# Optimization experiments

Hardware: AMD Instinct MI355X
Metric: run time of the kernel (lower is better)

The kernel has to match this reference:

```python
import jax, jax.numpy as jnp
import numpy as np

T, B, A, N = 64, 32, 8, 16
E, H = 64, 4
LSTM_I, LSTM_H = 128, 128
D_SELF = 16 + 9 * (32 - 2) + 4  # 290


def setup_inputs() -> dict:
    key = jax.random.key(0)
    ks = jax.random.split(key, 24)
    f32 = jnp.float32
    d = {}
    d["x_agent"] = jax.random.normal(ks[0], (T, B, A, 16), f32)
    d["x_lidar"] = jax.random.normal(ks[1], (T, B, A, 32), f32)
    d["x_safe_zone"] = jax.random.normal(ks[2], (T, B, A, 4), f32)
    d["x_ent0"] = jax.random.normal(ks[3], (T, B, A, N, 12), f32)
    d["x_ent1"] = jax.random.normal(ks[4], (T, B, A, N, 8), f32)
    d["mask0"] = jax.random.randint(ks[5], (T, B, A, N), 0, 2).astype(jnp.int32)
    d["mask1"] = jax.random.randint(ks[6], (T, B, A, N), 0, 2).astype(jnp.int32)
    d["done"] = jax.random.randint(ks[7], (T, B), 0, 2).astype(jnp.int32)
    d["actions"] = jax.random.randint(ks[8], (T, B, A, 2), 0, 5).astype(jnp.int32)
    w = lambda k, s: jax.random.normal(k, s, f32) * 0.05
    z = lambda s: jnp.zeros(s, f32)
    d["conv_w"] = w(ks[9], (9, 1, 3)); d["conv_b"] = z((9,))
    d["self_w"] = w(ks[10], (E, 2 * D_SELF)); d["self_b"] = z((E,))
    d["ent0_w"] = w(ks[11], (E, 12 + D_SELF)); d["ent0_b"] = z((E,))
    d["ent1_w"] = w(ks[12], (E, 8 + D_SELF)); d["ent1_b"] = z((E,))
    d["in_proj_w"] = w(ks[13], (3 * E, E)); d["in_proj_b"] = z((3 * E,))
    d["out_proj_w"] = w(ks[14], (E, E)); d["out_proj_b"] = z((E,))
    d["sa_w"] = w(ks[15], (E, E)); d["sa_b"] = z((E,))
    d["pool_w"] = w(ks[16], (LSTM_I, D_SELF + E)); d["pool_b"] = z((LSTM_I,))
    d["w_ih"] = w(ks[17], (4 * LSTM_H, LSTM_I)); d["w_hh"] = w(ks[18], (4 * LSTM_H, LSTM_H))
    d["b_ih"] = z((4 * LSTM_H,)); d["b_hh"] = z((4 * LSTM_H,))
    d["head0_w"] = w(ks[19], (5, LSTM_H)); d["head0_b"] = z((5,))
    d["head1_w"] = w(ks[20], (5, LSTM_H)); d["head1_b"] = z((5,))
    return d


def _forward(x_agent, x_lidar, x_safe_zone, x_ent0, x_ent1,
             conv_w, conv_b, self_w, self_b, ent0_w, ent0_b, ent1_w, ent1_b,
             in_proj_w, in_proj_b, out_proj_w, out_proj_b, sa_w, sa_b,
             pool_w, pool_b, w_ih, w_hh, b_ih, b_hh,
             head0_w, head0_b, head1_w, head1_b,
             mask0, mask1, done, actions):
    f32 = jnp.float32
    lin = lambda x, w, b: x @ w.T + b
    # lidar conv: Conv1d(1,9,k=3), padding=0 (padding_mode='circular' is inert with padding=0)
    xl = x_lidar.reshape(T * B * A, 1, 32)
    zl = jax.lax.conv_general_dilated(xl, conv_w, (1,), 'VALID',
                                      dimension_numbers=('NCH', 'OIH', 'NCH'))
    zl = jax.nn.relu(zl + conv_b[None, :, None]).reshape(T, B, A, -1)  # (T,B,A,270)
    x_self = jnp.concatenate([x_agent, zl, x_safe_zone], axis=-1)  # (T,B,A,290)
    z_self = jax.nn.relu(lin(jnp.concatenate([x_self, x_self], -1), self_w, self_b))[..., None, :]
    xs = jnp.broadcast_to(x_self[..., None, :], (T, B, A, N, D_SELF))
    z0 = jax.nn.relu(lin(jnp.concatenate([x_ent0, xs], -1), ent0_w, ent0_b))
    z1 = jax.nn.relu(lin(jnp.concatenate([x_ent1, xs], -1), ent1_w, ent1_b))
    z_ent = jnp.concatenate([z_self, z0, z1], axis=-2)  # (T,B,A,M,E), M = 1+2N = 33
    M = z_ent.shape[-2]
    mask = jnp.concatenate([jnp.ones((T, B, A, 1), f32),
                            mask0.astype(f32), mask1.astype(f32)], axis=-1)  # (T,B,A,M)
    # self-attention over entities, flattened over (T,B,A)
    S = T * B * A
    zf = z_ent.reshape(S, M, E)
    q, k, v = jnp.split(zf @ in_proj_w.T + in_proj_b, 3, axis=-1)
    Dh = E // H
    q = q.reshape(S, M, H, Dh); k = k.reshape(S, M, H, Dh); v = v.reshape(S, M, H, Dh)
    sc = jnp.einsum('sqhd,skhd->shqk', q, k) / np.float32(np.sqrt(Dh))
    valid = mask.reshape(S, M) > 0
    sc = jnp.where(valid[:, None, None, :], sc, jnp.float32(-1e9))
    attn = jax.nn.softmax(sc, axis=-1)
    o = jnp.einsum('shqk,skhd->sqhd', attn, v).reshape(S, M, E)
    o = (o @ out_proj_w.T + out_proj_b).reshape(T, B, A, M, E)
    res = z_ent + jax.nn.relu(lin(o, sa_w, sa_b))
    z_pool = jnp.mean(res * mask[..., None], axis=-2)  # torch.mean over entity dim (divide by M)
    zin = jax.nn.relu(lin(jnp.concatenate([x_self, z_pool], -1), pool_w, pool_b))  # (T,B,A,128)
    # LSTM scan with done-based state resets (PyTorch gate order i,f,g,o)
    zin_f = zin.reshape(T, B * A, LSTM_I)
    done_f = jnp.repeat(done.astype(f32), A, axis=-1)  # (T, B*A)
    def step(carry, inp):
        h, c = carry
        x_t, d_t = inp
        keep = (1.0 - d_t)[:, None]
        h = h * keep
        c = c * keep
        g = x_t @ w_ih.T + b_ih + h @ w_hh.T + b_hh
        i, f, gg, og = jnp.split(g, 4, axis=-1)
        c = jax.nn.sigmoid(f) * c + jax.nn.sigmoid(i) * jnp.tanh(gg)
        h = jax.nn.sigmoid(og) * jnp.tanh(c)
        return (h, c), h
    h0 = jnp.zeros((B * A, LSTM_H), f32)
    c0 = jnp.zeros((B * A, LSTM_H), f32)
    _, hs = jax.lax.scan(step, (h0, c0), (zin_f, done_f))
    z_lstm = hs.reshape(T, B, A, LSTM_H)
    # categorical heads: per-head logprob of given action and entropy
    lps, ents = [], []
    for i, (hw, hb) in enumerate(((head0_w, head0_b), (head1_w, head1_b))):
        logp = jax.nn.log_softmax(lin(z_lstm, hw, hb), axis=-1)
        p = jnp.exp(logp)
        ents.append(-(p * logp).sum(-1))
        lps.append(jnp.take_along_axis(logp, actions[..., i:i + 1], axis=-1)[..., 0])
    logprobs = lps[0] * lps[1]  # .prod(dim=-1) over heads as in source
    entropies = jnp.stack(ents, axis=-1)
    return logprobs, entropies


def reference(x_agent, x_lidar, x_safe_zone, x_ent0, x_ent1, mask0, mask1, done, actions,
              conv_w, conv_b, self_w, self_b, ent0_w, ent0_b, ent1_w, ent1_b,
              in_proj_w, in_proj_b, out_proj_w, out_proj_b, sa_w, sa_b,
              pool_w, pool_b, w_ih, w_hh, b_ih, b_hh,
              head0_w, head0_b, head1_w, head1_b):
    logprobs, entropies = _forward(x_agent, x_lidar, x_safe_zone, x_ent0, x_ent1,
                                   conv_w, conv_b, self_w, self_b, ent0_w, ent0_b,
                                   ent1_w, ent1_b, in_proj_w, in_proj_b, out_proj_w,
                                   out_proj_b, sa_w, sa_b, pool_w, pool_b,
                                   w_ih, w_hh, b_ih, b_hh,
                                   head0_w, head0_b, head1_w, head1_b,
                                   mask0, mask1, done, actions)
    return (actions, logprobs, entropies)
```

## Files before the change

### kernel.cpp

```cpp
#include <hip/hip_runtime.h>
#include <hip/hip_bf16.h>
#include <math.h>

#define T_DIM 64
#define B_DIM 32
#define S_TOT 16384
#define BA 256
#define FN_SB 16

#define ACT_OFF 0
#define LP_OFF 32768
#define ENT_OFF 49152

typedef __attribute__((ext_vector_type(8))) short short8;
typedef __attribute__((ext_vector_type(4))) float f32x4;
typedef unsigned int uint32;

__device__ __forceinline__ float sigf(float x) { return 1.0f / (1.0f + expf(-x)); }
__device__ __forceinline__ float bf2f(unsigned short u) {
    union { unsigned int i; float f; } a; a.i = ((unsigned int)u) << 16; return a.f;
}
__device__ __forceinline__ uint32 pkbf(float a, float b) {
    __hip_bfloat16 ha = __float2bfloat16(a), hb = __float2bfloat16(b);
    return (uint32)(*(unsigned short*)&ha) | ((uint32)(*(unsigned short*)&hb) << 16);
}
__device__ __forceinline__ short f2bs(float v) {
    __hip_bfloat16 h = __float2bfloat16(v); return *(short*)&h;
}
__device__ __forceinline__ int pswz(int row) { return (((row & 3) ^ ((row >> 2) & 3)) << 4); }

__global__ __launch_bounds__(256) void k_cvt2(
    const float* __restrict__ inp_w, const float* __restrict__ outp_w,
    const float* __restrict__ outp_b, const float* __restrict__ sa_w,
    const float* __restrict__ sa_b, const float* __restrict__ self_w,
    const float* __restrict__ pool_w, const float* __restrict__ ent0_w,
    const float* __restrict__ ent1_w, const float* __restrict__ w_ih,
    const float* __restrict__ w_hh,
    short* __restrict__ wq, short* __restrict__ Wf,
    short* __restrict__ We0, short* __restrict__ We1,
    short* __restrict__ wos, float* __restrict__ bos,
    short* __restrict__ wihb, short* __restrict__ whhb)
{
    int i = blockIdx.x * 256 + threadIdx.x;
    if (i < 12288) wq[i] = f2bs(inp_w[i]);
    if (i < 65536) { wihb[i] = f2bs(w_ih[i]); whhb[i] = f2bs(w_hh[i]); }
    if (i < 4096) {
        int c = i >> 6, k = i & 63;
        float s = 0.f;
        for (int j = 0; j < 64; ++j) s = fmaf(sa_w[c * 64 + j], outp_w[j * 64 + k], s);
        wos[i] = f2bs(s);
    }
    if (i < 64) {
        float s = sa_b[i];
        for (int j = 0; j < 64; ++j) s = fmaf(sa_w[i * 64 + j], outp_b[j], s);
        bos[i] = s;
    }
    if (i < 1024) {
        int e = i >> 4, k = i & 15;
        We0[i] = f2bs(k < 12 ? ent0_w[e * 302 + k] : 0.f);
        We1[i] = f2bs(k < 8 ? ent1_w[e * 298 + k] : 0.f);
    }
    if (i < 102400) {
        int c = i / 320, k = i - c * 320;
        float v = 0.f;
        if (k < 290) {
            if (c < 64) v = self_w[c * 580 + k] + self_w[c * 580 + 290 + k];
            else if (c < 192) v = pool_w[(size_t)(c - 64) * 354 + k];
            else if (c < 256) v = ent0_w[(c - 192) * 302 + 12 + k];
            else v = ent1_w[(c - 256) * 298 + 8 + k];
        }
        Wf[i] = f2bs(v);
    }
}

#define FN_XSB 0
#define FN_XP0 16384
#define FN_XP1 20736
#define FN_TOTAL 25088

__global__ __launch_bounds__(256, 4) void k_frontN(
    const float* __restrict__ xag, const float* __restrict__ xlid,
    const float* __restrict__ xsz, const float* __restrict__ xe0,
    const float* __restrict__ xe1,
    const float* __restrict__ conv_w, const float* __restrict__ conv_b,
    const float* __restrict__ self_b, const float* __restrict__ ent0_b,
    const float* __restrict__ ent1_b,
    const short* __restrict__ Wf, const short* __restrict__ We0,
    const short* __restrict__ We1,
    __hip_bfloat16* __restrict__ z_ent, float* __restrict__ zin_x)
{
    extern __shared__ char smem[];
    char* xsb = smem + FN_XSB;
    float* xp0f = (float*)(smem + FN_XP0);
    float* xp1f = (float*)(smem + FN_XP1);
    char* ae = smem + FN_XSB;
    float* lidf = (float*)(smem + FN_XP0);

    const int tid = threadIdx.x;
    const int s0 = blockIdx.x * FN_SB;
    const int wv = __builtin_amdgcn_readfirstlane(tid >> 6);
    const int l = tid & 63;
    const int lr = l & 15;
    const int lg = l >> 4;

    for (int i = tid; i < FN_SB * 32; i += 256) {
        int d = i & 31, sl = i >> 5;
        lidf[d * 18 + sl] = xlid[(size_t)s0 * 32 + i];
    }
    for (int i = tid; i < FN_SB * 16; i += 256) {
        int sl = i >> 4, d = i & 15;
        *(short*)(xsb + ((sl * 640 + d * 2) ^ ((sl & 7) << 4))) = f2bs(xag[(size_t)s0 * 16 + i]);
    }
    for (int i = tid; i < FN_SB * 4; i += 256) {
        int sl = i >> 2, d = i & 3;
        *(short*)(xsb + ((sl * 640 + (286 + d) * 2) ^ ((sl & 7) << 4))) = f2bs(xsz[(size_t)s0 * 4 + i]);
    }
    for (int i = tid; i < FN_SB * 30; i += 256) {
        int sl = i / 30, d = 290 + (i - (i / 30) * 30);
        *(short*)(xsb + ((sl * 640 + d * 2) ^ ((sl & 7) << 4))) = 0;
    }
    __syncthreads();
    for (int i = tid; i < 270 * FN_SB; i += 256) {
        int cp = i >> 4, sl = i & 15;
        int c = cp / 30, p = cp - c * 30;
        float v = conv_b[c] + conv_w[c * 3] * lidf[p * 18 + sl]
                + conv_w[c * 3 + 1] * lidf[(p + 1) * 18 + sl]
                + conv_w[c * 3 + 2] * lidf[(p + 2) * 18 + sl];
        *(short*)(xsb + ((sl * 640 + (16 + cp) * 2) ^ ((sl & 7) << 4))) = f2bs(fmaxf(v, 0.f));
    }
    __syncthreads();

    f32x4 acc[5];
    #pragma unroll
    for (int c = 0; c < 5; ++c) acc[c] = (f32x4){0.f, 0.f, 0.f, 0.f};

    for (int kk = 0; kk < 10; ++kk) {
        short8 af = *(const short8*)(xsb + ((lr * 640 + kk * 64 + lg * 16) ^ ((lr & 7) << 4)));
        short8 bf[5];
        #pragma unroll
        for (int c = 0; c < 5; ++c) {
            int col = (wv * 5 + c) * 16 + lr;
            bf[c] = *(const short8*)(Wf + (size_t)col * 320 + kk * 32 + lg * 8);
        }
        #pragma unroll
        for (int c = 0; c < 5; ++c)
            acc[c] = __builtin_amdgcn_mfma_f32_16x16x32_bf16(af, bf[c], acc[c], 0, 0, 0);
    }

    #pragma unroll
    for (int c = 0; c < 5; ++c) {
        int ct = wv * 5 + c;
        int gc = ct * 16 + lr;
        int rowb = lg * 4;
        f32x4 a = acc[c];
        if (ct * 16 < 64) {
            float bias = self_b[gc];
            #pragma unroll
            for (int r = 0; r < 4; ++r)
                z_ent[(size_t)(s0 + rowb + r) * 2112 + gc] = __float2bfloat16(fmaxf(a[r] + bias, 0.f));
        } else if (ct * 16 < 192) {
            int r2 = gc - 64;
            #pragma unroll
            for (int r = 0; r < 4; ++r)
                zin_x[(size_t)(s0 + rowb + r) * 128 + r2] = a[r];
        } else if (ct * 16 < 256) {
            float bias = ent0_b[gc - 192];
            #pragma unroll
            for (int r = 0; r < 4; ++r)
                xp0f[(rowb + r) * 68 + (gc - 192)] = a[r] + bias;
        } else {
            float bias = ent1_b[gc - 256];
            #pragma unroll
            for (int r = 0; r < 4; ++r)
                xp1f[(rowb + r) * 68 + (gc - 256)] = a[r] + bias;
        }
    }
    __syncthreads();

    {
        short8 bz = {0, 0, 0, 0, 0, 0, 0, 0};
        short8 be[4];
        #pragma unroll
        for (int ct = 0; ct < 4; ++ct) {
            int col = ct * 16 + lr;
            short8 bv = *(const short8*)(We0 + col * 16 + (lg & 1) * 8);
            be[ct] = (lg < 2) ? bv : bz;
        }
        for (int i = tid; i < 4096; i += 256) ((uint32*)ae)[i] = 0;
        __syncthreads();
        for (int i = tid; i < FN_SB * 192; i += 256) {
            int sl = i / 192, r = i - sl * 192;
            int n = r / 12, d = r - n * 12;
            int lrow = sl * 16 + n;
            *(short*)(ae + ((lrow * 64 + d * 2) ^ ((lrow & 3) << 4))) =
                f2bs(xe0[(size_t)s0 * 192 + i]);
        }
        __syncthreads();
        #pragma unroll
        for (int j = 0; j < 4; ++j) {
            int gs = wv * 4 + j;
            int row = gs * 16 + lr;
            short8 af = *(const short8*)(ae + ((row * 64 + lg * 16) ^ ((row & 3) << 4)));
            #pragma unroll
            for (int ct = 0; ct < 4; ++ct) {
                f32x4 a2 = {0.f, 0.f, 0.f, 0.f};
                a2 = __builtin_amdgcn_mfma_f32_16x16x32_bf16(af, be[ct], a2, 0, 0, 0);
                int e = ct * 16 + lr;
                float xpv = xp0f[gs * 68 + e];
                #pragma unroll
                for (int r = 0; r < 4; ++r) {
                    int n = lg * 4 + r;
                    z_ent[(size_t)(s0 + gs) * 2112 + (1 + n) * 64 + e] =
                        __float2bfloat16(fmaxf(a2[r] + xpv, 0.f));
                }
            }
        }
        __syncthreads();
    }

    {
        short8 bz = {0, 0, 0, 0, 0, 0, 0, 0};
        short8 be[4];
        #pragma unroll
        for (int ct = 0; ct < 4; ++ct) {
            int col = ct * 16 + lr;
            short8 bv = *(const short8*)(We1 + col * 16 + (lg & 1) * 8);
            be[ct] = (lg < 2) ? bv : bz;
        }
        for (int i = tid; i < 4096; i += 256) ((uint32*)ae)[i] = 0;
        __syncthreads();
        for (int i = tid; i < FN_SB * 128; i += 256) {
            int sl = i >> 7, r = i & 127;
            int n = r >> 3, d = r & 7;
            int lrow = sl * 16 + n;
            *(short*)(ae + ((lrow * 64 + d * 2) ^ ((lrow & 3) << 4))) =
                f2bs(xe1[(size_t)s0 * 128 + i]);
        }
        __syncthreads();
        #pragma unroll
        for (int j = 0; j < 4; ++j) {
            int gs = wv * 4 + j;
            int row = gs * 16 + lr;
            short8 af = *(const short8*)(ae + ((row * 64 + lg * 16) ^ ((row & 3) << 4)));
            #pragma unroll
            for (int ct = 0; ct < 4; ++ct) {
                f32x4 a2 = {0.f, 0.f, 0.f, 0.f};
                a2 = __builtin_amdgcn_mfma_f32_16x16x32_bf16(af, be[ct], a2, 0, 0, 0);
                int e = ct * 16 + lr;
                float xpv = xp1f[gs * 68 + e];
                #pragma unroll
                for (int r = 0; r < 4; ++r) {
                    int n = lg * 4 + r;
                    z_ent[(size_t)(s0 + gs) * 2112 + (17 + n) * 64 + e] =
                        __float2bfloat16(fmaxf(a2[r] + xpv, 0.f));
                }
            }
        }
    }
}

#define AG_QB   0
#define AG_KB   4224
#define AG_VT   8448
#define AG_PW   12544
#define AG_P32  16640
#define AG_V32  17408
#define AG_MSK  17664
#define AG_POOL 17824
#define AG_TOTAL 18080

__global__ __launch_bounds__(256, 8) void k_attnG(
    const __hip_bfloat16* __restrict__ z_ent, const float* __restrict__ zin_x_ws,
    const int* __restrict__ mask0, const int* __restrict__ mask1,
    const short* __restrict__ wqkvb, const float* __restrict__ inp_b,
    const short* __restrict__ wos_g, const float* __restrict__ bos_g,
    const float* __restrict__ pool_w, const float* __restrict__ pool_b,
    short* __restrict__ zinb)
{
    extern __shared__ char smem[];
    char*  Qb  = smem + AG_QB;
    char*  Kb  = smem + AG_KB;
    char*  Vt  = smem + AG_VT;
    char*  Pw  = smem + AG_PW;
    float* P32 = (float*)(smem + AG_P32);
    float* V32 = (float*)(smem + AG_V32);
    float* msk = (float*)(smem + AG_MSK);
    float* pooled = (float*)(smem + AG_POOL);
    char*  ob  = Qb;

    const int tid = threadIdx.x;
    const int s = blockIdx.x;
    const short* zg = (const short*)(z_ent + (size_t)s * 2112);

    if (tid < 16) msk[1 + tid] = (float)mask0[(size_t)s * 16 + tid];
    else if (tid < 32) msk[17 + (tid - 16)] = (float)mask1[(size_t)s * 16 + (tid - 16)];
    else if (tid == 32) msk[0] = 1.0f;
    __syncthreads();

    const int wv = __builtin_amdgcn_readfirstlane(tid >> 6);
    const int l  = tid & 63;
    const int lr = l & 15;
    const int lg = l >> 4;

    {
        short8 bw[3][2]; float bias[3];
        #pragma unroll
        for (int c = 0; c < 3; ++c) {
            int col = (wv * 3 + c) * 16 + lr;
            bw[c][0] = *(const short8*)(wqkvb + col * 64 + lg * 8);
            bw[c][1] = *(const short8*)(wqkvb + col * 64 + 32 + lg * 8);
            bias[c] = inp_b[col];
        }
        for (int rt = 0; rt < 3; ++rt) {
            int arow = rt * 16 + lr;
            short8 a0 = *(const short8*)(zg + arow * 64 + lg * 8);
            short8 a1 = *(const short8*)(zg + arow * 64 + 32 + lg * 8);
            #pragma unroll
            for (int c = 0; c < 3; ++c) {
                f32x4 acc = {0.f, 0.f, 0.f, 0.f};
                acc = __builtin_amdgcn_mfma_f32_16x16x32_bf16(a0, bw[c][0], acc, 0, 0, 0);
                acc = __builtin_amdgcn_mfma_f32_16x16x32_bf16(a1, bw[c][1], acc, 0, 0, 0);
                int col = (wv * 3 + c) * 16 + lr;
                int rb = rt * 16 + lg * 4;
                #pragma unroll
                for (int r = 0; r < 4; ++r) {
                    int q = rb + r;
                    if (q < 33) {
                        float val = acc[r] + bias[c];
                        if (col < 64) {
                            int h = col >> 4, d = col & 15;
                            *(short*)(Qb + ((h * 33 + q) * 32) + d * 2) = f2bs(val);
                        } else if (col < 128) {
                            int kc = col - 64; int h = kc >> 4, d = kc & 15;
                            *(short*)(Kb + ((h * 33 + q) * 32) + d * 2) = f2bs(val);
                        } else {
                            int vc = col - 128; int h = vc >> 4, d = vc & 15;
                            if (q < 32)
                                *(short*)(Vt + (h * 16 + d) * 64 + ((q * 2) ^ pswz(d))) = f2bs(val);
                            else
                                V32[h * 16 + d] = val;
                        }
                    }
                }
            }
        }
    }
    __syncthreads();

    uint32 pk[3][4];
    {
        const short8 zero8 = {0, 0, 0, 0, 0, 0, 0, 0};
        short8 kf[3];
        #pragma unroll
        for (int t = 0; t < 3; ++t)
            kf[t] = (lg < 2) ? *(const short8*)(Kb + ((wv * 33 + t * 16 + lr) * 32) + lg * 16) : zero8;
        float mk0 = msk[lr];
        float mk1 = msk[16 + lr];
        float mk2 = (lr == 0) ? msk[32] : 0.f;
        #pragma unroll
        for (int qt = 0; qt < 3; ++qt) {
            short8 qf = (lg < 2) ? *(const short8*)(Qb + ((wv * 33 + qt * 16 + lr) * 32) + lg * 16) : zero8;
            f32x4 z = {0.f, 0.f, 0.f, 0.f};
            f32x4 S0 = __builtin_amdgcn_mfma_f32_16x16x32_bf16(qf, kf[0], z, 0, 0, 0);
            f32x4 S1 = __builtin_amdgcn_mfma_f32_16x16x32_bf16(qf, kf[1], z, 0, 0, 0);
            f32x4 S2 = __builtin_amdgcn_mfma_f32_16x16x32_bf16(qf, kf[2], z, 0, 0, 0);
            #pragma unroll
            for (int r = 0; r < 4; ++r) {
                float v0 = (mk0 > 0.f) ? S0[r] * 0.25f : -1e9f;
                float v1 = (mk1 > 0.f) ? S1[r] * 0.25f : -1e9f;
                float v2 = (mk2 > 0.f) ? S2[r] * 0.25f : -1e9f;
                float m = fmaxf(fmaxf(v0, v1), v2);
                m = fmaxf(m, __shfl_xor(m, 1));
                m = fmaxf(m, __shfl_xor(m, 2));
                m = fmaxf(m, __shfl_xor(m, 4));
                m = fmaxf(m, __shfl_xor(m, 8));
                float e0 = __expf(v0 - m), e1 = __expf(v1 - m), e2 = __expf(v2 - m);
                float sm = e0 + e1 + e2;
                sm += __shfl_xor(sm, 1);
                sm += __shfl_xor(sm, 2);
                sm += __shfl_xor(sm, 4);
                sm += __shfl_xor(sm, 8);
                float inv = 1.0f / sm;
                pk[qt][r] = pkbf(e0 * inv, e1 * inv);
                if (lr == 0) P32[wv * 48 + qt * 16 + lg * 4 + r] = e2 * inv;
            }
        }
    }
    __syncthreads();

    {
        short8 vf = *(const short8*)(Vt + (wv * 16 + lr) * 64 + ((lg * 16) ^ pswz(lr)));
        float v32reg = V32[wv * 16 + lr];
        f32x4 C[3];
        #pragma unroll
        for (int qt = 0; qt < 3; ++qt) {
            #pragma unroll
            for (int r = 0; r < 4; ++r) {
                int ql = lg * 4 + r;
                uint32 p = pk[qt][r];
                char* prow = Pw + wv * 1024 + ql * 64;
                int sz = pswz(ql);
                *(short*)(prow + ((lr * 2) ^ sz)) = (short)(p & 0xffffu);
                *(short*)(prow + (((16 + lr) * 2) ^ sz)) = (short)(p >> 16);
            }
            short8 pf = *(const short8*)(Pw + wv * 1024 + lr * 64 + ((lg * 16) ^ pswz(lr)));
            f32x4 z = {0.f, 0.f, 0.f, 0.f};
            C[qt] = __builtin_amdgcn_mfma_f32_16x16x32_bf16(pf, vf, z, 0, 0, 0);
        }
        #pragma unroll
        for (int qt = 0; qt < 3; ++qt) {
            #pragma unroll
            for (int r = 0; r < 4; ++r) {
                int q = qt * 16 + lg * 4 + r;
                if (q <= 32) {
                    float cv = C[qt][r] + P32[wv * 48 + q] * v32reg;
                    *(short*)(ob + ((q * 128 + (wv * 16 + lr) * 2) ^ ((q & 7) << 4))) = f2bs(cv);
                }
            }
        }
    }
    __syncthreads();

    {
        int col = wv * 16 + lr;
        short8 b0 = *(const short8*)(wos_g + col * 64 + lg * 8);
        short8 b1 = *(const short8*)(wos_g + col * 64 + 32 + lg * 8);
        float bias = bos_g[col];
        float ps = 0.f;
        for (int rt = 0; rt < 3; ++rt) {
            int arow = rt * 16 + lr;
            int sw = (arow & 7) << 4;
            short8 a0 = *(const short8*)(ob + ((arow * 128 + lg * 16) ^ sw));
            short8 a1 = *(const short8*)(ob + ((arow * 128 + 64 + lg * 16) ^ sw));
            f32x4 acc = {0.f, 0.f, 0.f, 0.f};
            acc = __builtin_amdgcn_mfma_f32_16x16x32_bf16(a0, b0, acc, 0, 0, 0);
            acc = __builtin_amdgcn_mfma_f32_16x16x32_bf16(a1, b1, acc, 0, 0, 0);
            int rb = rt * 16 + lg * 4;
            #pragma unroll
            for (int r = 0; r < 4; ++r) {
                int row = rb + r;
                if (row < 33) {
                    float zev = bf2f(*(const unsigned short*)(zg + row * 64 + col));
                    ps += msk[row] * (zev + fmaxf(acc[r] + bias, 0.f));
                }
            }
        }
        ps += __shfl_xor(ps, 16); ps += __shfl_xor(ps, 32);
        if (lg == 0) pooled[col] = ps * (1.0f / 33.0f);
    }
    __syncthreads();

    if (tid < 128) {
        int r = tid;
        float acc = pool_b[r] + zin_x_ws[(size_t)s * 128 + r];
        const float* wrow = pool_w + (size_t)r * 354 + 290;
        #pragma unroll 8
        for (int e = 0; e < 64; ++e) acc = fmaf(wrow[e], pooled[e], acc);
        zinb[(size_t)s * 128 + r] = f2bs(fmaxf(acc, 0.f));
    }
}

__global__ __launch_bounds__(256, 2) void k_xproj(
    const short* __restrict__ zinb, const short* __restrict__ wihb,
    const float* __restrict__ b_ih, const float* __restrict__ b_hh,
    short* __restrict__ xp)
{
    extern __shared__ char smem[];
    char* at = smem;
    const int tid = threadIdx.x;
    const size_t r0 = (size_t)blockIdx.x * 64;

    for (int i = tid; i < 64 * 64; i += 256) {
        int row = i >> 6, dw = i & 63;
        uint32 v = ((const uint32*)(zinb + (r0 + row) * 128))[dw];
        *(uint32*)(at + ((row * 256 + dw * 4) ^ ((row & 7) << 4))) = v;
    }
    __syncthreads();

    const int wv = __builtin_amdgcn_readfirstlane(tid >> 6);
    const int l = tid & 63;
    const int lr = l & 15;
    const int lg = l >> 4;

    short8 af[4][4];
    #pragma unroll
    for (int rt = 0; rt < 4; ++rt)
        #pragma unroll
        for (int kc = 0; kc < 4; ++kc) {
            int row = rt * 16 + lr;
            af[rt][kc] = *(const short8*)(at + ((row * 256 + kc * 64 + lg * 16) ^ ((row & 7) << 4)));
        }

    for (int ct8 = 0; ct8 < 8; ++ct8) {
        int ct = wv * 8 + ct8;
        int col = ct * 16 + lr;
        short8 bf[4];
        #pragma unroll
        for (int kc = 0; kc < 4; ++kc)
            bf[kc] = *(const short8*)(wihb + (size_t)col * 128 + kc * 32 + lg * 8);
        float bias = b_ih[col] + b_hh[col];
        int g = col >> 7, j = col & 127;
        #pragma unroll
        for (int rt = 0; rt < 4; ++rt) {
            f32x4 acc = {0.f, 0.f, 0.f, 0.f};
            #pragma unroll
            for (int kc = 0; kc < 4; ++kc)
                acc = __builtin_amdgcn_mfma_f32_16x16x32_bf16(af[rt][kc], bf[kc], acc, 0, 0, 0);
            #pragma unroll
            for (int r = 0; r < 4; ++r)
                xp[(r0 + rt * 16 + lg * 4 + r) * 512 + j * 4 + g] = f2bs(acc[r] + bias);
        }
    }
}

__global__ __launch_bounds__(512, 1) void k_lstm2(
    const short* __restrict__ xp, const short* __restrict__ whhb,
    const int* __restrict__ done, float* __restrict__ h_all)
{
    __shared__ short hl[16 * 128];
    __shared__ float keepl[64 * 16];
    const int tid = threadIdx.x;
    const int s0 = blockIdx.x * 16;
    const int wv = __builtin_amdgcn_readfirstlane(tid >> 6);
    const int l = tid & 63;
    const int lr = l & 15;
    const int lg = l >> 4;

    for (int i = tid; i < 1024; i += 512) {
        int t = i >> 4, ls = i & 15;
        keepl[i] = done[t * 32 + ((s0 + ls) >> 3)] ? 0.f : 1.f;
    }
    for (int i = tid; i < 1024; i += 512) ((uint32*)hl)[i] = 0;

    short8 bf[4][4];
    #pragma unroll
    for (int gi = 0; gi < 4; ++gi) {
        int col = (gi * 8 + wv) * 16 + lr;
        #pragma unroll
        for (int kc = 0; kc < 4; ++kc)
            bf[gi][kc] = *(const short8*)(whhb + (size_t)col * 128 + kc * 32 + lg * 8);
    }
    float c0 = 0.f, c1 = 0.f, c2 = 0.f, c3 = 0.f;
    const int jcol = wv * 16 + lr;

    short4 xn[4];
    #pragma unroll
    for (int r = 0; r < 4; ++r)
        xn[r] = *(const short4*)(xp + ((size_t)(s0 + lg * 4 + r)) * 512 + jcol * 4);
    __syncthreads();

    for (int t = 0; t < T_DIM; ++t) {
        short4 xc[4];
        #pragma unroll
        for (int r = 0; r < 4; ++r) xc[r] = xn[r];
        if (t < 63) {
            #pragma unroll
            for (int r = 0; r < 4; ++r)
                xn[r] = *(const short4*)(xp + ((size_t)(t + 1) * 256 + s0 + lg * 4 + r) * 512 + jcol * 4);
        }
        short8 af[4];
        #pragma unroll
        for (int kc = 0; kc < 4; ++kc)
            af[kc] = *(const short8*)((char*)hl + ((lr * 256 + kc * 64 + lg * 16) ^ ((lr & 7) << 4)));
        f32x4 z = {0.f, 0.f, 0.f, 0.f};
        f32x4 Ci = z, Cf = z, Cg = z, Co = z;
        #pragma unroll
        for (int kc = 0; kc < 4; ++kc) {
            Ci = __builtin_amdgcn_mfma_f32_16x16x32_bf16(af[kc], bf[0][kc], Ci, 0, 0, 0);
            Cf = __builtin_amdgcn_mfma_f32_16x16x32_bf16(af[kc], bf[1][kc], Cf, 0, 0, 0);
            Cg = __builtin_amdgcn_mfma_f32_16x16x32_bf16(af[kc], bf[2][kc], Cg, 0, 0, 0);
            Co = __builtin_amdgcn_mfma_f32_16x16x32_bf16(af[kc], bf[3][kc], Co, 0, 0, 0);
        }
        __syncthreads();

        #pragma unroll
        for (int r = 0; r < 4; ++r) {
            int sl = lg * 4 + r;
            float kt = keepl[t * 16 + sl];
            float gi = bf2f((unsigned short)xc[r].x) + Ci[r];
            float gf = bf2f((unsigned short)xc[r].y) + Cf[r];
            float gg = bf2f((unsigned short)xc[r].z) + Cg[r];
            float go = bf2f((unsigned short)xc[r].w) + Co[r];
            float cc = (r == 0 ? c0 : r == 1 ? c1 : r == 2 ? c2 : c3) * kt;
            cc = sigf(gf) * cc + sigf(gi) * tanhf(gg);
            float hn = sigf(go) * tanhf(cc);
            if (r == 0) c0 = cc; else if (r == 1) c1 = cc; else if (r == 2) c2 = cc; else c3 = cc;
            float kn = (t < 63) ? keepl[(t + 1) * 16 + sl] : 1.f;
            *(short*)((char*)hl + ((sl * 256 + jcol * 2) ^ ((sl & 7) << 4))) = f2bs(hn * kn);
            h_all[((size_t)t * 256 + s0 + sl) * 128 + jcol] = hn;
        }
        __syncthreads();
    }
}

__global__ __launch_bounds__(256) void k_heads(
    const float* __restrict__ h_all, const int* __restrict__ actions,
    const float* __restrict__ h0w, const float* __restrict__ h0b,
    const float* __restrict__ h1w, const float* __restrict__ h1b,
    float* __restrict__ out)
{
    __shared__ float w0[640], w1[640], b0[8], b1[8];
    const int tid = threadIdx.x;
    for (int i = tid; i < 640; i += 256) { w0[i] = h0w[i]; w1[i] = h1w[i]; }
    if (tid < 5) { b0[tid] = h0b[tid]; b1[tid] = h1b[tid]; }
    __syncthreads();
    const int g = blockIdx.x * 256 + tid;
    const float* h = h_all + (size_t)g * 128;
    float l0[5], l1[5];
    #pragma unroll
    for (int cc = 0; cc < 5; ++cc) { l0[cc] = b0[cc]; l1[cc] = b1[cc]; }
    for (int j = 0; j < 128; ++j) {
        float hv = h[j];
        #pragma unroll
        for (int cc = 0; cc < 5; ++cc) {
            l0[cc] = fmaf(w0[cc * 128 + j], hv, l0[cc]);
            l1[cc] = fmaf(w1[cc * 128 + j], hv, l1[cc]);
        }
    }
    int a0 = actions[(size_t)g * 2], a1 = actions[(size_t)g * 2 + 1];
    float m0 = l0[0], m1 = l1[0];
    #pragma unroll
    for (int cc = 1; cc < 5; ++cc) { m0 = fmaxf(m0, l0[cc]); m1 = fmaxf(m1, l1[cc]); }
    float s0 = 0.f, s1 = 0.f;
    #pragma unroll
    for (int cc = 0; cc < 5; ++cc) { s0 += expf(l0[cc] - m0); s1 += expf(l1[cc] - m1); }
    float lse0 = m0 + logf(s0), lse1 = m1 + logf(s1);
    float ent0 = 0.f, ent1 = 0.f, lp0 = 0.f, lp1 = 0.f;
    #pragma unroll
    for (int cc = 0; cc < 5; ++cc) {
        float p0 = l0[cc] - lse0, p1 = l1[cc] - lse1;
        ent0 -= expf(p0) * p0;
        ent1 -= expf(p1) * p1;
        if (cc == a0) lp0 = p0;
        if (cc == a1) lp1 = p1;
    }
    out[ACT_OFF + (size_t)g * 2]     = (float)a0;
    out[ACT_OFF + (size_t)g * 2 + 1] = (float)a1;
    out[LP_OFF + g]                  = lp0 * lp1;
    out[ENT_OFF + (size_t)g * 2]     = ent0;
    out[ENT_OFF + (size_t)g * 2 + 1] = ent1;
}

extern "C" void kernel_launch(void* const* d_in, const int* in_sizes, int n_in,
                              void* d_out, int out_size, void* d_ws, size_t ws_size,
                              hipStream_t stream)
{
    const float* x_agent = (const float*)d_in[0];
    const float* x_lidar = (const float*)d_in[1];
    const float* x_safe  = (const float*)d_in[2];
    const float* x_ent0  = (const float*)d_in[3];
    const float* x_ent1  = (const float*)d_in[4];
    const int*   mask0   = (const int*)d_in[5];
    const int*   mask1   = (const int*)d_in[6];
    const int*   done    = (const int*)d_in[7];
    const int*   actions = (const int*)d_in[8];
    const float* conv_w  = (const float*)d_in[9];
    const float* conv_b  = (const float*)d_in[10];
    const float* self_w  = (const float*)d_in[11];
    const float* self_b  = (const float*)d_in[12];
    const float* ent0_w  = (const float*)d_in[13];
    const float* ent0_b  = (const float*)d_in[14];
    const float* ent1_w  = (const float*)d_in[15];
    const float* ent1_b  = (const float*)d_in[16];
    const float* inp_w   = (const float*)d_in[17];
    const float* inp_b   = (const float*)d_in[18];
    const float* outp_w  = (const float*)d_in[19];
    const float* outp_b  = (const float*)d_in[20];
    const float* sa_w    = (const float*)d_in[21];
    const float* sa_b    = (const float*)d_in[22];
    const float* pool_w  = (const float*)d_in[23];
    const float* pool_b  = (const float*)d_in[24];
    const float* w_ih    = (const float*)d_in[25];
    const float* w_hh    = (const float*)d_in[26];
    const float* b_ih    = (const float*)d_in[27];
    const float* b_hh    = (const float*)d_in[28];
    const float* h0w     = (const float*)d_in[29];
    const float* h0b     = (const float*)d_in[30];
    const float* h1w     = (const float*)d_in[31];
    const float* h1b     = (const float*)d_in[32];

    __hip_bfloat16* z_ent = (__hip_bfloat16*)d_ws;
    float* zin_x = (float*)((char*)d_ws + (size_t)S_TOT * 2112 * 2);
    short* zinb  = (short*)(zin_x + (size_t)S_TOT * 128);
    float* h_all = (float*)(zinb + (size_t)S_TOT * 128);
    short* xp    = (short*)(h_all + (size_t)S_TOT * 128);
    short* wqkvb = xp + (size_t)S_TOT * 512;
    short* Wf    = wqkvb + 12288;
    short* We0   = Wf + 102400;
    short* We1   = We0 + 1024;
    short* wos   = We1 + 1024;
    float* bos   = (float*)(wos + 4096);
    short* wihb  = (short*)(bos + 64);
    short* whhb  = wihb + 65536;

    k_cvt2<<<400, 256, 0, stream>>>(inp_w, outp_w, outp_b, sa_w, sa_b, self_w, pool_w,
                                    ent0_w, ent1_w, w_ih, w_hh,
                                    wqkvb, Wf, We0, We1, wos, bos, wihb, whhb);

    k_frontN<<<S_TOT / FN_SB, 256, FN_TOTAL, stream>>>(
        x_agent, x_lidar, x_safe, x_ent0, x_ent1,
        conv_w, conv_b, self_b, ent0_b, ent1_b,
        Wf, We0, We1, z_ent, zin_x);

    k_attnG<<<S_TOT, 256, AG_TOTAL, stream>>>(
        z_ent, zin_x, mask0, mask1, wqkvb, inp_b, wos, bos,
        pool_w, pool_b, zinb);

    k_xproj<<<256, 256, 16384, stream>>>(zinb, wihb, b_ih, b_hh, xp);

    k_lstm2<<<16, 512, 0, stream>>>(xp, whhb, done, h_all);

    k_heads<<<S_TOT / 256, 256, 0, stream>>>(h_all, actions, h0w, h0b, h1w, h1b, (float*)d_out);
}
```

Before: 371.4 us.

## Move pooled projection out of attention into MFMA input-projection kernel; pack entity stores

Removes the per-sample scalar pool_w projection tail (a 64-wide dot product per output row, read from fp32 global weights) from the attention kernel. The attention kernel now writes the pooled vectors to a workspace, and a fused k_zinx kernel computes the projection with bf16 MFMA before feeding the LSTM input projection. The entity-encoder weights are permuted so each lane holds two adjacent columns, which lets z_ent be written with packed 32-bit bf16 stores. It also drops a barrier and clamps the attention row index. In exchange it adds a pooled workspace round-trip through global memory and a bf16 rounding of pooled before the projection.

After: 341.9 us. 7.9% less time.

```diff
diff --git a/kernel.cpp b/kernel.cpp
--- a/kernel.cpp
+++ b/kernel.cpp
@@ -39,11 +39,13 @@
     short* __restrict__ wq, short* __restrict__ Wf,
     short* __restrict__ We0, short* __restrict__ We1,
     short* __restrict__ wos, float* __restrict__ bos,
-    short* __restrict__ wihb, short* __restrict__ whhb)
+    short* __restrict__ wihb, short* __restrict__ whhb,
+    short* __restrict__ wp2)
 {
     int i = blockIdx.x * 256 + threadIdx.x;
     if (i < 12288) wq[i] = f2bs(inp_w[i]);
     if (i < 65536) { wihb[i] = f2bs(w_ih[i]); whhb[i] = f2bs(w_hh[i]); }
+    if (i < 8192) { int c = i >> 6, k = i & 63; wp2[i] = f2bs(pool_w[(size_t)c * 354 + 290 + k]); }
     if (i < 4096) {
         int c = i >> 6, k = i & 63;
         float s = 0.f;
@@ -56,7 +58,9 @@
         bos[i] = s;
     }
     if (i < 1024) {
-        int e = i >> 4, k = i & 15;
+        int cp = i >> 4, k = i & 15;
+        int ct = cp >> 4, lr2 = cp & 15;
+        int e = 32 * (ct >> 1) + 2 * lr2 + (ct & 1);
         We0[i] = f2bs(k < 12 ? ent0_w[e * 302 + k] : 0.f);
         We1[i] = f2bs(k < 8 ? ent1_w[e * 298 + k] : 0.f);
     }
@@ -201,17 +205,23 @@
             int gs = wv * 4 + j;
             int row = gs * 16 + lr;
             short8 af = *(const short8*)(ae + ((row * 64 + lg * 16) ^ ((row & 3) << 4)));
+            f32x4 a2[4];
             #pragma unroll
             for (int ct = 0; ct < 4; ++ct) {
-                f32x4 a2 = {0.f, 0.f, 0.f, 0.f};
-                a2 = __builtin_amdgcn_mfma_f32_16x16x32_bf16(af, be[ct], a2, 0, 0, 0);
-                int e = ct * 16 + lr;
-                float xpv = xp0f[gs * 68 + e];
+                f32x4 z = {0.f, 0.f, 0.f, 0.f};
+                a2[ct] = __builtin_amdgcn_mfma_f32_16x16x32_bf16(af, be[ct], z, 0, 0, 0);
+            }
+            #pragma unroll
+            for (int t = 0; t < 2; ++t) {
+                int e0 = 32 * t + 2 * lr;
+                float xv0 = xp0f[gs * 68 + e0];
+                float xv1 = xp0f[gs * 68 + e0 + 1];
                 #pragma unroll
                 for (int r = 0; r < 4; ++r) {
                     int n = lg * 4 + r;
-                    z_ent[(size_t)(s0 + gs) * 2112 + (1 + n) * 64 + e] =
-                        __float2bfloat16(fmaxf(a2[r] + xpv, 0.f));
+                    float v0 = fmaxf(a2[2 * t][r] + xv0, 0.f);
+                    float v1 = fmaxf(a2[2 * t + 1][r] + xv1, 0.f);
+                    *(uint32*)((char*)z_ent + ((size_t)(s0 + gs) * 2112 + (1 + n) * 64 + e0) * 2) = pkbf(v0, v1);
                 }
             }
         }
@@ -242,17 +252,23 @@
             int gs = wv * 4 + j;
             int row = gs * 16 + lr;
             short8 af = *(const short8*)(ae + ((row * 64 + lg * 16) ^ ((row & 3) << 4)));
+            f32x4 a2[4];
             #pragma unroll
             for (int ct = 0; ct < 4; ++ct) {
-                f32x4 a2 = {0.f, 0.f, 0.f, 0.f};
-                a2 = __builtin_amdgcn_mfma_f32_16x16x32_bf16(af, be[ct], a2, 0, 0, 0);
-                int e = ct * 16 + lr;
-                float xpv = xp1f[gs * 68 + e];
+                f32x4 z = {0.f, 0.f, 0.f, 0.f};
+                a2[ct] = __builtin_amdgcn_mfma_f32_16x16x32_bf16(af, be[ct], z, 0, 0, 0);
+            }
+            #pragma unroll
+            for (int t = 0; t < 2; ++t) {
+                int e0 = 32 * t + 2 * lr;
+                float xv0 = xp1f[gs * 68 + e0];
+                float xv1 = xp1f[gs * 68 + e0 + 1];
                 #pragma unroll
                 for (int r = 0; r < 4; ++r) {
                     int n = lg * 4 + r;
-                    z_ent[(size_t)(s0 + gs) * 2112 + (17 + n) * 64 + e] =
-                        __float2bfloat16(fmaxf(a2[r] + xpv, 0.f));
+                    float v0 = fmaxf(a2[2 * t][r] + xv0, 0.f);
+                    float v1 = fmaxf(a2[2 * t + 1][r] + xv1, 0.f);
+                    *(uint32*)((char*)z_ent + ((size_t)(s0 + gs) * 2112 + (17 + n) * 64 + e0) * 2) = pkbf(v0, v1);
                 }
             }
         }
@@ -266,16 +282,14 @@
 #define AG_P32  16640
 #define AG_V32  17408
 #define AG_MSK  17664
-#define AG_POOL 17824
-#define AG_TOTAL 18080
+#define AG_TOTAL 17824
 
 __global__ __launch_bounds__(256, 8) void k_attnG(
-    const __hip_bfloat16* __restrict__ z_ent, const float* __restrict__ zin_x_ws,
+    const __hip_bfloat16* __restrict__ z_ent,
     const int* __restrict__ mask0, const int* __restrict__ mask1,
     const short* __restrict__ wqkvb, const float* __restrict__ inp_b,
     const short* __restrict__ wos_g, const float* __restrict__ bos_g,
-    const float* __restrict__ pool_w, const float* __restrict__ pool_b,
-    short* __restrict__ zinb)
+    float* __restrict__ pooled_ws)
 {
     extern __shared__ char smem[];
     char*  Qb  = smem + AG_QB;
@@ -285,7 +299,6 @@
     float* P32 = (float*)(smem + AG_P32);
     float* V32 = (float*)(smem + AG_V32);
     float* msk = (float*)(smem + AG_MSK);
-    float* pooled = (float*)(smem + AG_POOL);
     char*  ob  = Qb;
 
     const int tid = threadIdx.x;
@@ -295,7 +308,6 @@
     if (tid < 16) msk[1 + tid] = (float)mask0[(size_t)s * 16 + tid];
     else if (tid < 32) msk[17 + (tid - 16)] = (float)mask1[(size_t)s * 16 + (tid - 16)];
     else if (tid == 32) msk[0] = 1.0f;
-    __syncthreads();
 
     const int wv = __builtin_amdgcn_readfirstlane(tid >> 6);
     const int l  = tid & 63;
@@ -313,6 +325,7 @@
         }
         for (int rt = 0; rt < 3; ++rt) {
             int arow = rt * 16 + lr;
+            if (arow > 32) arow = 32;
             short8 a0 = *(const short8*)(zg + arow * 64 + lg * 8);
             short8 a1 = *(const short8*)(zg + arow * 64 + 32 + lg * 8);
             #pragma unroll
@@ -446,34 +459,26 @@
             }
         }
         ps += __shfl_xor(ps, 16); ps += __shfl_xor(ps, 32);
-        if (lg == 0) pooled[col] = ps * (1.0f / 33.0f);
-    }
-    __syncthreads();
-
-    if (tid < 128) {
-        int r = tid;
-        float acc = pool_b[r] + zin_x_ws[(size_t)s * 128 + r];
-        const float* wrow = pool_w + (size_t)r * 354 + 290;
-        #pragma unroll 8
-        for (int e = 0; e < 64; ++e) acc = fmaf(wrow[e], pooled[e], acc);
-        zinb[(size_t)s * 128 + r] = f2bs(fmaxf(acc, 0.f));
-    }
-}
-
-__global__ __launch_bounds__(256, 2) void k_xproj(
-    const short* __restrict__ zinb, const short* __restrict__ wihb,
-    const float* __restrict__ b_ih, const float* __restrict__ b_hh,
-    short* __restrict__ xp)
+        if (lg == 0) pooled_ws[(size_t)s * 64 + col] = ps * (1.0f / 33.0f);
+    }
+}
+
+__global__ __launch_bounds__(256, 2) void k_zinx(
+    const float* __restrict__ pooled_ws, const float* __restrict__ zin_x,
+    const short* __restrict__ wp2, const float* __restrict__ pool_b,
+    const short* __restrict__ wihb, const float* __restrict__ b_ih,
+    const float* __restrict__ b_hh, short* __restrict__ xp)
 {
     extern __shared__ char smem[];
-    char* at = smem;
+    char* A1 = smem;
+    char* zt = smem + 8192;
     const int tid = threadIdx.x;
     const size_t r0 = (size_t)blockIdx.x * 64;
 
-    for (int i = tid; i < 64 * 64; i += 256) {
-        int row = i >> 6, dw = i & 63;
-        uint32 v = ((const uint32*)(zinb + (r0 + row) * 128))[dw];
-        *(uint32*)(at + ((row * 256 + dw * 4) ^ ((row & 7) << 4))) = v;
+    for (int i = tid; i < 2048; i += 256) {
+        int sl = i >> 5, dp = i & 31;
+        float2 v = ((const float2*)(pooled_ws + (r0 + sl) * 64))[dp];
+        *(uint32*)(A1 + ((sl * 128 + dp * 4) ^ ((sl & 7) << 4))) = pkbf(v.x, v.y);
     }
     __syncthreads();
 
@@ -482,13 +487,37 @@
     const int lr = l & 15;
     const int lg = l >> 4;
 
+    #pragma unroll
+    for (int c = 0; c < 2; ++c) {
+        int col = (wv * 2 + c) * 16 + lr;
+        short8 bf0 = *(const short8*)(wp2 + col * 64 + lg * 8);
+        short8 bf1 = *(const short8*)(wp2 + col * 64 + 32 + lg * 8);
+        float bias = pool_b[col];
+        #pragma unroll
+        for (int rt = 0; rt < 4; ++rt) {
+            int row16 = rt * 16 + lr;
+            short8 a0 = *(const short8*)(A1 + ((row16 * 128 + lg * 16) ^ ((row16 & 7) << 4)));
+            short8 a1 = *(const short8*)(A1 + ((row16 * 128 + 64 + lg * 16) ^ ((row16 & 7) << 4)));
+            f32x4 acc = {0.f, 0.f, 0.f, 0.f};
+            acc = __builtin_amdgcn_mfma_f32_16x16x32_bf16(a0, bf0, acc, 0, 0, 0);
+            acc = __builtin_amdgcn_mfma_f32_16x16x32_bf16(a1, bf1, acc, 0, 0, 0);
+            #pragma unroll
+            for (int r = 0; r < 4; ++r) {
+                int row = rt * 16 + lg * 4 + r;
+                float v = fmaxf(acc[r] + bias + zin_x[(r0 + row) * 128 + col], 0.f);
+                *(short*)(zt + ((row * 256 + col * 2) ^ ((row & 7) << 4))) = f2bs(v);
+            }
+        }
+    }
+    __syncthreads();
+
     short8 af[4][4];
     #pragma unroll
     for (int rt = 0; rt < 4; ++rt)
         #pragma unroll
         for (int kc = 0; kc < 4; ++kc) {
             int row = rt * 16 + lr;
-            af[rt][kc] = *(const short8*)(at + ((row * 256 + kc * 64 + lg * 16) ^ ((row & 7) << 4)));
+            af[rt][kc] = *(const short8*)(zt + ((row * 256 + kc * 64 + lg * 16) ^ ((row & 7) << 4)));
         }
 
     for (int ct8 = 0; ct8 < 8; ++ct8) {
@@ -680,22 +709,23 @@
     const float* h1b     = (const float*)d_in[32];
 
     __hip_bfloat16* z_ent = (__hip_bfloat16*)d_ws;
-    float* zin_x = (float*)((char*)d_ws + (size_t)S_TOT * 2112 * 2);
-    short* zinb  = (short*)(zin_x + (size_t)S_TOT * 128);
-    float* h_all = (float*)(zinb + (size_t)S_TOT * 128);
-    short* xp    = (short*)(h_all + (size_t)S_TOT * 128);
-    short* wqkvb = xp + (size_t)S_TOT * 512;
-    short* Wf    = wqkvb + 12288;
-    short* We0   = Wf + 102400;
-    short* We1   = We0 + 1024;
-    short* wos   = We1 + 1024;
-    float* bos   = (float*)(wos + 4096);
-    short* wihb  = (short*)(bos + 64);
-    short* whhb  = wihb + 65536;
+    float* zin_x  = (float*)((char*)d_ws + (size_t)S_TOT * 2112 * 2);
+    float* pooled = zin_x + (size_t)S_TOT * 128;
+    float* h_all  = pooled + (size_t)S_TOT * 64;
+    short* xp     = (short*)(h_all + (size_t)S_TOT * 128);
+    short* wqkvb  = xp + (size_t)S_TOT * 512;
+    short* Wf     = wqkvb + 12288;
+    short* We0    = Wf + 102400;
+    short* We1    = We0 + 1024;
+    short* wos    = We1 + 1024;
+    float* bos    = (float*)(wos + 4096);
+    short* wihb   = (short*)(bos + 64);
+    short* whhb   = wihb + 65536;
+    short* wp2    = whhb + 65536;
 
     k_cvt2<<<400, 256, 0, stream>>>(inp_w, outp_w, outp_b, sa_w, sa_b, self_w, pool_w,
                                     ent0_w, ent1_w, w_ih, w_hh,
-                                    wqkvb, Wf, We0, We1, wos, bos, wihb, whhb);
+                                    wqkvb, Wf, We0, We1, wos, bos, wihb, whhb, wp2);
 
     k_frontN<<<S_TOT / FN_SB, 256, FN_TOTAL, stream>>>(
         x_agent, x_lidar, x_safe, x_ent0, x_ent1,
@@ -703,10 +733,9 @@
         Wf, We0, We1, z_ent, zin_x);
 
     k_attnG<<<S_TOT, 256, AG_TOTAL, stream>>>(
-        z_ent, zin_x, mask0, mask1, wqkvb, inp_b, wos, bos,
-        pool_w, pool_b, zinb);
-
-    k_xproj<<<256, 256, 16384, stream>>>(zinb, wihb, b_ih, b_hh, xp);
+        z_ent, mask0, mask1, wqkvb, inp_b, wos, bos, pooled);
+
+    k_zinx<<<256, 256, 24576, stream>>>(pooled, zin_x, wp2, pool_b, wihb, b_ih, b_hh, xp);
 
     k_lstm2<<<16, 512, 0, stream>>>(xp, whhb, done, h_all);
 
```
